# Kernel tuning notes

Measured on AMD Instinct MI355X. Metric: run time of the kernel, lower is better.

## Reference

```python
import jax, jax.numpy as jnp
import numpy as np
from jax import lax

# ---- module config (init_kwargs) ----
B, CIN, COUT, H, W, K = 16, 32, 32, 256, 256, 3
FEATURE_BITS = 8
INPUT_ZP = 3
OUTPUT_ZP = -5
INPUT_SCALE = 0.02
OUTPUT_SCALE = 0.05
STRIDE = (1, 1)
PAD_H, PAD_W = 1, 1
DILATION = (1, 1)
GROUPS = 1
QMIN, QMAX = -(2 ** (FEATURE_BITS - 1)), 2 ** (FEATURE_BITS - 1) - 1  # -128, 127


def float_to_fixed_point(scale, bitwidth):
    # Represent scale (in (0,1)) as int_scale * 2^-frac_bits with int_scale <= 2^(b-1)-1.
    # Pick the largest frac_bits s.t. round(scale * 2^frac_bits) fits -> max precision.
    qmax = jnp.float32(2 ** (bitwidth - 1) - 1)
    frac_bits = jnp.floor(jnp.log2(qmax / scale)).astype(jnp.int32)
    int_scale = jnp.round(scale * jnp.exp2(frac_bits.astype(jnp.float32))).astype(jnp.int32)
    return int_scale, frac_bits


def setup_inputs() -> dict:
    key = jax.random.key(0)
    k0, k1, k2, k3 = jax.random.split(key, 4)
    x = jax.random.randint(k0, (B, CIN, H, W), -128, 128, dtype=jnp.int32).astype(jnp.int8)
    qweight = jax.random.randint(k1, (COUT, CIN, K, K), -128, 128, dtype=jnp.int32).astype(jnp.int8)
    qbias = jax.random.randint(k2, (COUT,), -1000, 1000, dtype=jnp.int32)
    weight_scale = jax.random.uniform(k3, (COUT,), jnp.float32, 1e-3, 1e-2)
    return {"x": x, "qweight": qweight, "qbias": qbias, "weight_scale": weight_scale}


def reference(x, qweight, qbias, weight_scale):
    # F.pad(qinput, (pw,pw,ph,ph), 'constant', input_zero_point) -> pad W and H dims
    xp = jnp.pad(x, ((0, 0), (0, 0), (PAD_H, PAD_H), (PAD_W, PAD_W)),
                 mode="constant", constant_values=INPUT_ZP)
    # int32 conv (no bias), VALID since input was pre-padded
    out = lax.conv_general_dilated(
        xp.astype(jnp.int32), qweight.astype(jnp.int32),
        window_strides=STRIDE, padding="VALID", rhs_dilation=DILATION,
        dimension_numbers=("NCHW", "OIHW", "NCHW"), feature_group_count=GROUPS)
    # shifted bias: qbias - sum(qweight) * input_zero_point  (per out channel)
    shifted_qbias = qbias - qweight.astype(jnp.int32).sum((1, 2, 3)) * INPUT_ZP
    out = out + shifted_qbias[None, :, None, None]
    # fixed-point requant: (out * int_scale) >> frac_bits, per channel
    folded_scale = (INPUT_SCALE * weight_scale / OUTPUT_SCALE).astype(jnp.float32)
    int_scale, frac_bits = float_to_fixed_point(folded_scale, FEATURE_BITS)
    out = jnp.right_shift(out * int_scale[None, :, None, None],
                          frac_bits[None, :, None, None])  # arithmetic shift on int32
    out = out + OUTPUT_ZP
    out = jnp.clip(out, QMIN, QMAX).astype(jnp.int8)
    return out
```

## Files before the change

kernel.cpp:

```cpp
#include <hip/hip_runtime.h>

#define B_   16
#define CIN  32
#define COUT 32
#define H_   256
#define W_   256
#define IN_ZP  3
#define OUT_ZP (-5)
#define HW (H_ * W_)
#define TH 8
#define TW 64
#define SW 72
#define SH 10

using i32x4  = __attribute__((ext_vector_type(4))) int;
using i32x16 = __attribute__((ext_vector_type(16))) int;

__global__ void qconv_prep(const int* __restrict__ qw, const int* __restrict__ qb,
                           const float* __restrict__ wscale, int* __restrict__ ws) {
    const int co  = blockIdx.x;
    const int tid = threadIdx.x;
    __shared__ int red[4];
    const int* wco = qw + co * (CIN * 9);

    int s = 0;
    for (int i = tid; i < CIN * 9; i += 256) s += wco[i];
    for (int off = 32; off; off >>= 1) s += __shfl_down(s, off, 64);
    if ((tid & 63) == 0) red[tid >> 6] = s;

    if (tid < 72) {
        int gidx = blockIdx.x * 72 + tid;
        int g    = gidx & 3;
        int lane = (gidx >> 2) & 63;
        int t    = gidx >> 8;
        int wco2 = lane & 31;
        int ci0  = 16 * (lane >> 5) + 4 * g;
        const int* base = qw + wco2 * (CIN * 9);
        int b0 = base[(ci0 + 0) * 9 + t] & 0xff;
        int b1 = base[(ci0 + 1) * 9 + t] & 0xff;
        int b2 = base[(ci0 + 2) * 9 + t] & 0xff;
        int b3 = base[(ci0 + 3) * 9 + t] & 0xff;
        ws[gidx] = b0 | (b1 << 8) | (b2 << 16) | (b3 << 24);
    }
    __syncthreads();
    if (tid == 0) {
        int wsum = red[0] + red[1] + red[2] + red[3];
        ws[2304 + co] = qb[co] - wsum * IN_ZP;
        float fs = (0.02f * wscale[co]) / 0.05f;
        float fb = floorf(log2f(127.0f / fs));
        int isc = (int)rintf(fs * exp2f(fb));
        ws[2336 + co] = isc | (((int)fb) << 16);
    }
}

__device__ __forceinline__ void stage_item(int idx, int ht, int wt,
                                           const int* __restrict__ xb,
                                           int (*smem)[SH][SW]) {
    int cig = idx / 180;
    int rem = idx - cig * 180;
    int r   = rem / 18;
    int c4  = rem - r * 18;
    int gh  = ht - 1 + r;
    int gw0 = wt - 4 + c4 * 4;
    int ghc = min(H_ - 1, max(0, gh));
    int gwc = min(W_ - 4, max(0, gw0));
    const int* p = xb + (cig * 4) * HW + ghc * W_ + gwc;
    i32x4 v0 = *(const i32x4*)(p);
    i32x4 v1 = *(const i32x4*)(p + HW);
    i32x4 v2 = *(const i32x4*)(p + 2 * HW);
    i32x4 v3 = *(const i32x4*)(p + 3 * HW);
    bool vh = (unsigned)gh < (unsigned)H_;
    i32x4 pk;
#pragma unroll
    for (int j = 0; j < 4; ++j) {
        int t = (v0[j] & 0xff) | ((v1[j] & 0xff) << 8) |
                ((v2[j] & 0xff) << 16) | (v3[j] << 24);
        bool ok = vh && ((unsigned)(gw0 + j) < (unsigned)W_);
        pk[j] = ok ? t : 0x03030303;
    }
    *(i32x4*)&smem[cig][r][c4 * 4] = pk;
}

__global__ __launch_bounds__(256) void qconv_fused(const int* __restrict__ x,
                                                   const int* __restrict__ ws,
                                                   int* __restrict__ out) {
    __shared__ int smem[8][SH][SW];
    __shared__ __align__(16) int cons[64];

    const int d  = blockIdx.x + 4 * blockIdx.y + 128 * blockIdx.z;
    const int w  = ((d & 7) << 8) | (d >> 3);
    const int tx = w & 3;
    const int ty = (w >> 2) & 31;
    const int tb = w >> 7;

    const int wt = tx * TW;
    const int ht = ty * TH;
    const int tid = threadIdx.x;
    const int* xb = x + tb * (CIN * HW);

    if (tid < 64) cons[tid] = ws[2304 + tid];

    stage_item(tid,        ht, wt, xb, smem);
    stage_item(tid + 256,  ht, wt, xb, smem);
    stage_item(tid + 512,  ht, wt, xb, smem);
    stage_item(tid + 768,  ht, wt, xb, smem);
    stage_item(tid + 1024, ht, wt, xb, smem);
    if (tid < 160) stage_item(tid + 1280, ht, wt, xb, smem);
    __syncthreads();

    const int lane = tid & 63, wv = tid >> 6;
    const int hh  = lane >> 5;
    const int pix = lane & 31;

    i32x4 wfrag[9];
    const i32x4* wsv = (const i32x4*)ws;
#pragma unroll
    for (int t = 0; t < 9; ++t) wfrag[t] = wsv[t * 64 + lane];

#pragma unroll
    for (int i = 0; i < 4; ++i) {
        const int mt = wv * 4 + i;
        const int r0 = mt >> 1, chunk = mt & 1;
        i32x16 acc;
#pragma unroll
        for (int r = 0; r < 16; ++r) acc[r] = 0;
#pragma unroll
        for (int t = 0; t < 9; ++t) {
            const int dh = t / 3, dw = t % 3;
            const int rr = r0 + dh;
            const int c  = chunk * 32 + pix + dw + 3;
            i32x4 a;
#pragma unroll
            for (int g = 0; g < 4; ++g) a[g] = smem[4 * hh + g][rr][c];
            acc = __builtin_amdgcn_mfma_i32_32x32x32_i8(wfrag[t], a, acc, 0, 0, 0);
        }
        int* op = out + (tb * COUT) * HW + (ht + r0) * W_ + wt + chunk * 32 + pix;
#pragma unroll
        for (int rg = 0; rg < 4; ++rg) {
            const int cb = 4 * hh + 8 * rg;
            i32x4 sb4 = *(const i32x4*)&cons[cb];
            i32x4 qf4 = *(const i32x4*)&cons[32 + cb];
#pragma unroll
            for (int j = 0; j < 4; ++j) {
                int q = qf4[j];
                int v = acc[rg * 4 + j] + sb4[j];
                v = (int)((unsigned)v * (unsigned)(q & 0xffff)) >> (q >> 16);
                v += OUT_ZP;
                v = min(127, max(-128, v));
                op[(cb + j) * HW] = v;
            }
        }
    }
}

extern "C" void kernel_launch(void* const* d_in, const int* in_sizes, int n_in,
                              void* d_out, int out_size, void* d_ws, size_t ws_size,
                              hipStream_t stream) {
    const int*   x   = (const int*)d_in[0];
    const int*   qw  = (const int*)d_in[1];
    const int*   qb  = (const int*)d_in[2];
    const float* wsc = (const float*)d_in[3];
    int* ws  = (int*)d_ws;
    int* out = (int*)d_out;

    qconv_prep<<<32, 256, 0, stream>>>(qw, qb, wsc, ws);
    dim3 grid(W_ / TW, H_ / TH, B_);
    qconv_fused<<<grid, 256, 0, stream>>>(x, ws, out);
}
```

Measured before the change: 252.8 us.

## Pre-pack padded int8x4 input into workspace before the conv kernel

Adds a pack pass that converts the int32-stored input into a padded, channel-packed int8x4 layout in the workspace, fused with the weight/constant prep kernel. The main conv kernel then stages tiles with plain vector loads and no bounds checks or byte packing, reading a quarter of the bytes per tile. The cost is an extra full pass over the input (read int32, write packed) plus a second read of the packed buffer, and it depends on the workspace being large enough, otherwise the old path is used.

```diff
diff --git a/kernel.cpp b/kernel.cpp
--- a/kernel.cpp
+++ b/kernel.cpp
@@ -13,21 +13,186 @@
 #define SW 72
 #define SH 10
 
+#define XPH 258
+#define XPW 264
+#define XPQ 66
+#define PLANE_W (XPH * XPW)
+#define XP_WORDS (B_ * 8 * PLANE_W)
+#define WS_TAB 2400
+#define WS_NEED ((size_t)(WS_TAB + XP_WORDS) * 4)
+#define NQ (B_ * 8 * XPH * XPQ)
+#define PACK_BLOCKS 2176
+
 using i32x4  = __attribute__((ext_vector_type(4))) int;
 using i32x16 = __attribute__((ext_vector_type(16))) int;
 
-__global__ void qconv_prep(const int* __restrict__ qw, const int* __restrict__ qb,
-                           const float* __restrict__ wscale, int* __restrict__ ws) {
+
+__global__ __launch_bounds__(256) void qconv_pack(const int* __restrict__ x,
+                                                  const int* __restrict__ qw,
+                                                  const int* __restrict__ qb,
+                                                  const float* __restrict__ wscale,
+                                                  int* __restrict__ ws) {
+    const int bid = blockIdx.x;
+    const int tid = threadIdx.x;
+    if (bid < 32) {
+        __shared__ int red[4];
+        const int co = bid;
+        const int* wco = qw + co * (CIN * 9);
+        int s = 0;
+        for (int i = tid; i < CIN * 9; i += 256) s += wco[i];
+        for (int off = 32; off; off >>= 1) s += __shfl_down(s, off, 64);
+        if ((tid & 63) == 0) red[tid >> 6] = s;
+
+        if (tid < 72) {
+            int gidx = co * 72 + tid;
+            int g    = gidx & 3;
+            int lane = (gidx >> 2) & 63;
+            int t    = gidx >> 8;
+            int wco2 = lane & 31;
+            int ci0  = 16 * (lane >> 5) + 4 * g;
+            const int* base = qw + wco2 * (CIN * 9);
+            int b0 = base[(ci0 + 0) * 9 + t] & 0xff;
+            int b1 = base[(ci0 + 1) * 9 + t] & 0xff;
+            int b2 = base[(ci0 + 2) * 9 + t] & 0xff;
+            int b3 = base[(ci0 + 3) * 9 + t] & 0xff;
+            ws[gidx] = b0 | (b1 << 8) | (b2 << 16) | (b3 << 24);
+        }
+        __syncthreads();
+        if (tid == 0) {
+            int wsum = red[0] + red[1] + red[2] + red[3];
+            ws[2304 + co] = qb[co] - wsum * IN_ZP;
+            float fs = (0.02f * wscale[co]) / 0.05f;
+            float fb = floorf(log2f(127.0f / fs));
+            int isc = (int)rintf(fs * exp2f(fb));
+            ws[2336 + co] = isc | (((int)fb) << 16);
+        }
+        return;
+    }
+    int* __restrict__ xp = ws + WS_TAB;
+    const int T = (PACK_BLOCKS) * 256;
+    for (int q = (bid - 32) * 256 + tid; q < NQ; q += T) {
+        int b   = q / (8 * XPH * XPQ);
+        int r1  = q - b * (8 * XPH * XPQ);
+        int cig = r1 / (XPH * XPQ);
+        int r2  = r1 - cig * (XPH * XPQ);
+        int ph  = r2 / XPQ;
+        int cq  = r2 - ph * XPQ;
+        int gh  = ph - 1;
+        int gw0 = cq * 4 - 4;
+        int ghc = min(H_ - 1, max(0, gh));
+        int gwc = min(W_ - 4, max(0, gw0));
+        const int* p = x + (b * CIN + cig * 4) * HW + ghc * W_ + gwc;
+        i32x4 v0 = *(const i32x4*)(p);
+        i32x4 v1 = *(const i32x4*)(p + HW);
+        i32x4 v2 = *(const i32x4*)(p + 2 * HW);
+        i32x4 v3 = *(const i32x4*)(p + 3 * HW);
+        bool vh = (unsigned)gh < (unsigned)H_;
+        i32x4 pk;
+#pragma unroll
+        for (int j = 0; j < 4; ++j) {
+            int t = (v0[j] & 0xff) | ((v1[j] & 0xff) << 8) |
+                    ((v2[j] & 0xff) << 16) | (v3[j] << 24);
+            bool ok = vh && ((unsigned)(gw0 + j) < (unsigned)W_);
+            pk[j] = ok ? t : 0x03030303;
+        }
+        *(i32x4*)(xp + 4 * q) = pk;
+    }
+}
+
+__global__ __launch_bounds__(256) void qconv_fused(const int* __restrict__ ws,
+                                                   int* __restrict__ out) {
+    __shared__ int smem[8][SH][SW];
+    __shared__ __align__(16) int cons[64];
+
+    const int d  = blockIdx.x + 4 * blockIdx.y + 128 * blockIdx.z;
+    const int w  = ((d & 7) << 8) | (d >> 3);
+    const int tx = w & 3;
+    const int ty = (w >> 2) & 31;
+    const int tb = w >> 7;
+
+    const int wt = tx * TW;
+    const int ht = ty * TH;
+    const int tid = threadIdx.x;
+    const int* __restrict__ xp = ws + WS_TAB;
+
+    if (tid < 64) cons[tid] = ws[2304 + tid];
+
+    int* sl = &smem[0][0][0];
+    const int rowbase = (tb * 8) * XPH + ht;
+#define SRC_OF(idx_) (xp + ((rowbase + ((idx_) / 180) * XPH + ((idx_) % 180) / 18) * XPW \
+                            + wt + 4 * (((idx_) % 180) % 18)))
+    i32x4 v0 = *(const i32x4*)SRC_OF(tid);
+    i32x4 v1 = *(const i32x4*)SRC_OF(tid + 256);
+    i32x4 v2 = *(const i32x4*)SRC_OF(tid + 512);
+    i32x4 v3 = *(const i32x4*)SRC_OF(tid + 768);
+    i32x4 v4 = *(const i32x4*)SRC_OF(tid + 1024);
+    i32x4 v5 = {};
+    const bool tail = tid < 160;
+    if (tail) v5 = *(const i32x4*)SRC_OF(tid + 1280);
+    *(i32x4*)(sl + 4 * tid)          = v0;
+    *(i32x4*)(sl + 4 * (tid + 256))  = v1;
+    *(i32x4*)(sl + 4 * (tid + 512))  = v2;
+    *(i32x4*)(sl + 4 * (tid + 768))  = v3;
+    *(i32x4*)(sl + 4 * (tid + 1024)) = v4;
+    if (tail) *(i32x4*)(sl + 4 * (tid + 1280)) = v5;
+#undef SRC_OF
+    __syncthreads();
+
+    const int lane = tid & 63, wv = tid >> 6;
+    const int hh  = lane >> 5;
+    const int pix = lane & 31;
+
+    i32x4 wfrag[9];
+    const i32x4* wsv = (const i32x4*)ws;
+#pragma unroll
+    for (int t = 0; t < 9; ++t) wfrag[t] = wsv[t * 64 + lane];
+
+#pragma unroll
+    for (int i = 0; i < 4; ++i) {
+        const int mt = wv * 4 + i;
+        const int r0 = mt >> 1, chunk = mt & 1;
+        i32x16 acc;
+#pragma unroll
+        for (int r = 0; r < 16; ++r) acc[r] = 0;
+#pragma unroll
+        for (int t = 0; t < 9; ++t) {
+            const int dh = t / 3, dw = t % 3;
+            const int rr = r0 + dh;
+            const int c  = chunk * 32 + pix + dw + 3;
+            i32x4 a;
+#pragma unroll
+            for (int g = 0; g < 4; ++g) a[g] = smem[4 * hh + g][rr][c];
+            acc = __builtin_amdgcn_mfma_i32_32x32x32_i8(wfrag[t], a, acc, 0, 0, 0);
+        }
+        int* op = out + (tb * COUT) * HW + (ht + r0) * W_ + wt + chunk * 32 + pix;
+#pragma unroll
+        for (int rg = 0; rg < 4; ++rg) {
+            const int cb = 4 * hh + 8 * rg;
+            i32x4 sb4 = *(const i32x4*)&cons[cb];
+            i32x4 qf4 = *(const i32x4*)&cons[32 + cb];
+#pragma unroll
+            for (int j = 0; j < 4; ++j) {
+                int q = qf4[j];
+                int v = acc[rg * 4 + j] + sb4[j];
+                v = (int)((unsigned)v * (unsigned)(q & 0xffff)) >> (q >> 16);
+                v += OUT_ZP;
+                v = min(127, max(-128, v));
+                op[(cb + j) * HW] = v;
+            }
+        }
+    }
+}
+
+__global__ void qconv_prep_fb(const int* __restrict__ qw, const int* __restrict__ qb,
+                              const float* __restrict__ wscale, int* __restrict__ ws) {
     const int co  = blockIdx.x;
     const int tid = threadIdx.x;
     __shared__ int red[4];
     const int* wco = qw + co * (CIN * 9);
-
     int s = 0;
     for (int i = tid; i < CIN * 9; i += 256) s += wco[i];
     for (int off = 32; off; off >>= 1) s += __shfl_down(s, off, 64);
     if ((tid & 63) == 0) red[tid >> 6] = s;
-
     if (tid < 72) {
         int gidx = blockIdx.x * 72 + tid;
         int g    = gidx & 3;
@@ -81,25 +246,21 @@
     *(i32x4*)&smem[cig][r][c4 * 4] = pk;
 }
 
-__global__ __launch_bounds__(256) void qconv_fused(const int* __restrict__ x,
-                                                   const int* __restrict__ ws,
-                                                   int* __restrict__ out) {
+__global__ __launch_bounds__(256) void qconv_fused_fb(const int* __restrict__ x,
+                                                      const int* __restrict__ ws,
+                                                      int* __restrict__ out) {
     __shared__ int smem[8][SH][SW];
     __shared__ __align__(16) int cons[64];
-
     const int d  = blockIdx.x + 4 * blockIdx.y + 128 * blockIdx.z;
     const int w  = ((d & 7) << 8) | (d >> 3);
     const int tx = w & 3;
     const int ty = (w >> 2) & 31;
     const int tb = w >> 7;
-
     const int wt = tx * TW;
     const int ht = ty * TH;
     const int tid = threadIdx.x;
     const int* xb = x + tb * (CIN * HW);
-
     if (tid < 64) cons[tid] = ws[2304 + tid];
-
     stage_item(tid,        ht, wt, xb, smem);
     stage_item(tid + 256,  ht, wt, xb, smem);
     stage_item(tid + 512,  ht, wt, xb, smem);
@@ -107,16 +268,13 @@
     stage_item(tid + 1024, ht, wt, xb, smem);
     if (tid < 160) stage_item(tid + 1280, ht, wt, xb, smem);
     __syncthreads();
-
     const int lane = tid & 63, wv = tid >> 6;
     const int hh  = lane >> 5;
     const int pix = lane & 31;
-
     i32x4 wfrag[9];
     const i32x4* wsv = (const i32x4*)ws;
 #pragma unroll
     for (int t = 0; t < 9; ++t) wfrag[t] = wsv[t * 64 + lane];
-
 #pragma unroll
     for (int i = 0; i < 4; ++i) {
         const int mt = wv * 4 + i;
@@ -162,8 +320,13 @@
     const float* wsc = (const float*)d_in[3];
     int* ws  = (int*)d_ws;
     int* out = (int*)d_out;
-
-    qconv_prep<<<32, 256, 0, stream>>>(qw, qb, wsc, ws);
     dim3 grid(W_ / TW, H_ / TH, B_);
-    qconv_fused<<<grid, 256, 0, stream>>>(x, ws, out);
-}
+
+    if (ws_size >= WS_NEED) {
+        qconv_pack<<<32 + PACK_BLOCKS, 256, 0, stream>>>(x, qw, qb, wsc, ws);
+        qconv_fused<<<grid, 256, 0, stream>>>(ws, out);
+    } else {
+        qconv_prep_fb<<<32, 256, 0, stream>>>(qw, qb, wsc, ws);
+        qconv_fused_fb<<<grid, 256, 0, stream>>>(x, ws, out);
+    }
+}
```

Result: no change. 253.8 us (+0.4%).
